# Kernel optimization log

Measured on AMD Instinct MI355X. Metric: run time of the kernel, lower is better.

## Reference

```python
import jax, jax.numpy as jnp
import numpy as np

GAMMAS = (0.01, 0.1, 1.0, 10.0, 100.0)
FOCAL_GAMMA = 2.0
SMOOTH = 0.1
TASK_W = (0.4, 0.3, 0.3)
A_RECON, A_ORTH, A_ADV = 1.0, 0.1, 0.1
NUM_DOMAINS = 4
NUM_LABELS1 = 4


def focal_smooth(logits, targets, maskf):
    # FocalLoss.forward with smoothing > 0, masked mean
    n_classes = logits.shape[1]
    log_p = jax.nn.log_softmax(logits, axis=1)
    p = jnp.exp(log_p)
    onehot = jax.nn.one_hot(targets, n_classes, dtype=logits.dtype)
    smooth = onehot * (1.0 - SMOOTH) + SMOOTH / n_classes
    ce = -(smooth * log_p).sum(axis=1)
    pt = jnp.take_along_axis(p, targets[:, None], axis=1)[:, 0]
    loss = ce * (1.0 - pt) ** FOCAL_GAMMA
    return (loss * maskf).sum() / jnp.maximum(maskf.sum(), 1.0)


def ce_masked(logits, targets, maskf):
    log_p = jax.nn.log_softmax(logits, axis=1)
    nll = -jnp.take_along_axis(log_p, targets[:, None], axis=1)[:, 0]
    return (nll * maskf).sum() / jnp.maximum(maskf.sum(), 1.0)


def cond_mmd(feats, domains, labels, maskf):
    # Global pairwise sq-distance matrix; multi-gamma RBF kernels summed.
    sq = (feats ** 2).sum(axis=-1)                      # (B,)
    Dmat = sq[:, None] + sq[None, :] - 2.0 * feats @ feats.T  # (B,B)
    Ksum = jnp.zeros_like(Dmat)
    for g in GAMMAS:
        Ksum = Ksum + jnp.exp(-g * Dmat)
    loss = jnp.asarray(0.0, feats.dtype)
    count = jnp.asarray(0.0, feats.dtype)
    for lab in range(NUM_LABELS1):
        lm = (labels == lab).astype(feats.dtype) * maskf
        for d1 in range(NUM_DOMAINS):
            m1 = lm * (domains == d1).astype(feats.dtype)
            n1 = m1.sum()
            Km1 = Ksum @ m1
            for d2 in range(d1 + 1, NUM_DOMAINS):
                m2 = lm * (domains == d2).astype(feats.dtype)
                n2 = m2.sum()
                valid = (n1 > 1) & (n2 > 1)
                term = (m1 @ Km1) / jnp.maximum(n1, 1.0) ** 2 \
                     + (m2 @ (Ksum @ m2)) / jnp.maximum(n2, 1.0) ** 2 \
                     - 2.0 * (m2 @ Km1) / jnp.maximum(n1 * n2, 1.0)
                loss = loss + jnp.where(valid, term, 0.0)
                count = count + valid.astype(feats.dtype)
    return loss / jnp.maximum(count, 1.0)


def hsic(c, s):
    n = c.shape[0]
    c = c / jnp.maximum(jnp.linalg.norm(c, axis=-1, keepdims=True), 1e-12)
    s = s / jnp.maximum(jnp.linalg.norm(s, axis=-1, keepdims=True), 1e-12)
    K = c @ c.T
    L = s @ s.T
    Kc = K - K.mean(axis=0, keepdims=True) - K.mean(axis=1, keepdims=True) + K.mean()
    Lc = L - L.mean(axis=0, keepdims=True) - L.mean(axis=1, keepdims=True) + L.mean()
    return (Kc * Lc).sum() / (n - 1) ** 2


def setup_inputs() -> dict:
    key = jax.random.key(0)
    ks = jax.random.split(key, 20)
    B, D, H = 4096, 256, 768
    inp = {
        'logits1': jax.random.normal(ks[0], (B, 4), jnp.float32),
        'labels1': jax.random.randint(ks[1], (B,), 0, 4),
        'logits2': jax.random.normal(ks[2], (B, 6), jnp.float32),
        'labels2': jax.random.randint(ks[3], (B,), 0, 6),
        'logits3': jax.random.normal(ks[4], (B, 3), jnp.float32),
        'labels3': jax.random.randint(ks[5], (B,), 0, 3),
        'c_v': jax.random.normal(ks[6], (B, D), jnp.float32),
        's_v': jax.random.normal(ks[7], (B, D), jnp.float32),
        'c_t': jax.random.normal(ks[8], (B, D), jnp.float32),
        's_t': jax.random.normal(ks[9], (B, D), jnp.float32),
        'v_sv': jax.random.normal(ks[10], (B, NUM_DOMAINS), jnp.float32),
        'v_st': jax.random.normal(ks[11], (B, NUM_DOMAINS), jnp.float32),
        'domain_labels': jax.random.randint(ks[12], (B,), 0, NUM_DOMAINS),
        'mask': jnp.ones((B,), dtype=bool),
        'h_img_recon': jax.random.normal(ks[13], (B, H), jnp.float32),
        'h_img_orig': jax.random.normal(ks[14], (B, H), jnp.float32),
        'h_txt_recon': jax.random.normal(ks[15], (B, H), jnp.float32),
        'h_txt_orig': jax.random.normal(ks[16], (B, H), jnp.float32),
    }
    return inp


def reference(logits1, labels1, logits2, labels2, logits3, labels3,
              c_v, s_v, c_t, s_t, v_sv, v_st, domain_labels, mask,
              h_img_recon, h_img_orig, h_txt_recon, h_txt_orig):
    maskf = mask.astype(jnp.float32)
    total = jnp.asarray(0.0, jnp.float32)
    # classification (focal + label smoothing), per-task weighted
    total = total + TASK_W[0] * focal_smooth(logits1, labels1, maskf)
    total = total + TASK_W[1] * focal_smooth(logits2, labels2, maskf)
    total = total + TASK_W[2] * focal_smooth(logits3, labels3, maskf)
    # adversarial: CE on spurious domain logits + conditional MMD on causal feats
    l_adv_s = ce_masked(v_sv, domain_labels, maskf) + ce_masked(v_st, domain_labels, maskf)
    l_adv_c = cond_mmd(c_v, domain_labels, labels1, maskf) \
            + cond_mmd(c_t, domain_labels, labels1, maskf)
    total = total + A_ADV * (l_adv_s + l_adv_c)
    # orthogonality (HSIC), on unmasked features as in source
    l_orth = hsic(c_v, s_v) + hsic(c_t, s_t)
    total = total + A_ORTH * l_orth
    # reconstruction MSE
    l_recon = jnp.mean((h_img_recon - h_img_orig) ** 2) + jnp.mean((h_txt_recon - h_txt_orig) ** 2)
    total = total + A_RECON * l_recon
    return total
```

## Files before the change

### kernel.cpp

```cpp
#include <hip/hip_runtime.h>
#include <hip/hip_bf16.h>


typedef short bf16x8 __attribute__((ext_vector_type(8)));
typedef float f32x4 __attribute__((ext_vector_type(4)));
typedef unsigned long long u64;
typedef unsigned int u32;

static constexpr int D = 256;
static constexpr int H = 768;
static constexpr int NG = 16;
static constexpr float FX32 = 4294967296.f;
static constexpr float IFX32 = 2.3283064365386963e-10f;

__device__ inline void gAddFx(u64* p, float v) {
  long long q = (long long)llroundf(v * FX32);
  atomicAdd(p, (u64)q);
}
__device__ inline float fxToF(u64 v) { return (float)(long long)v * IFX32; }

__device__ inline float focal_n(const float* x, int n, int tgt,
                                float s_over_n, float oms) {
  float mx = x[0];
  for (int c = 1; c < n; ++c) mx = fmaxf(mx, x[c]);
  float se = 0.f, sx = 0.f;
  for (int c = 0; c < n; ++c) { se += __expf(x[c] - mx); sx += x[c]; }
  float logZ = mx + __logf(se);
  float ce = logZ - oms * x[tgt] - s_over_n * sx;
  float pt = __expf(x[tgt] - logZ);
  float om = 1.f - pt;
  return ce * om * om;
}

extern "C" __global__ __launch_bounds__(256) void k_pre(
    const void* __restrict__ mask, const int* __restrict__ y1,
    const int* __restrict__ dom,
    const float* __restrict__ l1, const float* __restrict__ l2,
    const float* __restrict__ l3, const int* __restrict__ y2,
    const int* __restrict__ y3,
    const float* __restrict__ vsv, const float* __restrict__ vst,
    const float* __restrict__ cv, const float* __restrict__ sv,
    const float* __restrict__ ct, const float* __restrict__ st,
    const float* __restrict__ ir, const float* __restrict__ io,
    const float* __restrict__ trc, const float* __restrict__ to,
    u64* SA, u64* GCU, u64* U64,
    int* gid, float* sq, float* inv, unsigned short* bf, u32* CNTB,
    int B, int N4, int NA, int NB) {
  __shared__ u32 sh3[3];
  __shared__ u32 cnt[17];
  __shared__ int redi[4];
  __shared__ float redf[4];
  __shared__ float redf5[5][4];
  __shared__ float ub[4][64][4];
  int bid = blockIdx.x;
  int t = threadIdx.x;

  if (bid < NA) {
    if (t < 3) sh3[t] = 0;
    if (t < 17) cnt[t] = 0;
    __syncthreads();
    u32 a = 0, b2 = 0, cd = 0;
    if (t * 16 + 15 < B) {
      uint4 wv = ((const uint4*)mask)[t];
      u32 ws[4] = {wv.x, wv.y, wv.z, wv.w};
      #pragma unroll
      for (int j = 0; j < 4; ++j) {
        a |= ws[j] & 0xffu; b2 |= ws[j] & 0xff00u; cd |= ws[j] & 0xffff0000u;
      }
    }
    if (a) atomicOr(&sh3[0], 1u);
    if (b2) atomicOr(&sh3[1], 1u);
    if (cd) atomicOr(&sh3[2], 1u);
    __syncthreads();
    int mode;
    if ((sh3[1] | sh3[2]) == 0) mode = 0;
    else if (sh3[0] == 0 && sh3[1] == 0) mode = 1;
    else mode = 2;
    int r = bid * 256 + t;
    int mi = 0;
    float s[5] = {0.f, 0.f, 0.f, 0.f, 0.f};
    if (r < B) {
      if (mode == 0)      mi = ((const int*)mask)[r] ? 1 : 0;
      else if (mode == 1) mi = (((const float*)mask)[r] != 0.f) ? 1 : 0;
      else                mi = ((const unsigned char*)mask)[r] ? 1 : 0;
      int g = -1;
      if (mi) { g = y1[r] * 4 + dom[r]; atomicAdd(&cnt[g], 1u); }
      else atomicAdd(&cnt[16], 1u);
      gid[r] = g;
      if (mi) {
        float x[6];
        for (int c = 0; c < 4; ++c) x[c] = l1[r * 4 + c];
        s[0] = focal_n(x, 4, y1[r], 0.1f / 4.f, 0.9f);
        for (int c = 0; c < 6; ++c) x[c] = l2[r * 6 + c];
        s[1] = focal_n(x, 6, y2[r], 0.1f / 6.f, 0.9f);
        for (int c = 0; c < 3; ++c) x[c] = l3[r * 3 + c];
        s[2] = focal_n(x, 3, y3[r], 0.1f / 3.f, 0.9f);
        int d = dom[r];
        for (int c = 0; c < 4; ++c) x[c] = vsv[r * 4 + c];
        {
          float mx = fmaxf(fmaxf(x[0], x[1]), fmaxf(x[2], x[3]));
          float se = __expf(x[0]-mx)+__expf(x[1]-mx)+__expf(x[2]-mx)+__expf(x[3]-mx);
          s[3] = mx + __logf(se) - x[d];
        }
        for (int c = 0; c < 4; ++c) x[c] = vst[r * 4 + c];
        {
          float mx = fmaxf(fmaxf(x[0], x[1]), fmaxf(x[2], x[3]));
          float se = __expf(x[0]-mx)+__expf(x[1]-mx)+__expf(x[2]-mx)+__expf(x[3]-mx);
          s[4] = mx + __logf(se) - x[d];
        }
      }
    }
    int v = mi;
    #pragma unroll
    for (int o = 32; o > 0; o >>= 1) {
      v += __shfl_down(v, o);
      #pragma unroll
      for (int k = 0; k < 5; ++k) s[k] += __shfl_down(s[k], o);
    }
    if ((t & 63) == 0) {
      redi[t >> 6] = v;
      #pragma unroll
      for (int k = 0; k < 5; ++k) redf5[k][t >> 6] = s[k];
    }
    __syncthreads();
    if (t == 0) {
      atomicAdd(&SA[5], (u64)(redi[0] + redi[1] + redi[2] + redi[3]));
      #pragma unroll
      for (int k = 0; k < 5; ++k)
        gAddFx(&SA[k], redf5[k][0] + redf5[k][1] + redf5[k][2] + redf5[k][3]);
    }
    if (t < NG && cnt[t]) atomicAdd(&GCU[t], (u64)cnt[t]);
    if (t < 17) CNTB[bid * 17 + t] = cnt[t];
  } else if (bid < NA + NB) {
    int b = bid - NA;
    int perF = NB >> 2;
    int f = b / perF;
    int rb = b - f * perF;
    const float* p = (f == 0) ? cv : (f == 1) ? sv : (f == 2) ? ct : st;
    int w = t >> 6, L = t & 63;
    float up0 = 0.f, up1 = 0.f, up2 = 0.f, up3 = 0.f;
    for (int bt = 0; bt < 2; ++bt) {
      int rbase = rb * 32 + w * 8 + bt * 4;
      float4 vv[4];
      #pragma unroll
      for (int i = 0; i < 4; ++i)
        vv[i] = ((const float4*)(p + (size_t)(rbase + i) * D))[L];
      float ss[4];
      #pragma unroll
      for (int i = 0; i < 4; ++i)
        ss[i] = vv[i].x * vv[i].x + vv[i].y * vv[i].y
              + vv[i].z * vv[i].z + vv[i].w * vv[i].w;
      #pragma unroll
      for (int o = 32; o > 0; o >>= 1) {
        #pragma unroll
        for (int i = 0; i < 4; ++i) ss[i] += __shfl_down(ss[i], o);
      }
      #pragma unroll
      for (int i = 0; i < 4; ++i) ss[i] = __shfl(ss[i], 0);
      #pragma unroll
      for (int i = 0; i < 4; ++i) {
        int r = rbase + i;
        float iv = 1.f / fmaxf(sqrtf(ss[i]), 1e-12f);
        if ((f & 1) == 0) {
          int fi = f >> 1;
          alignas(8) __hip_bfloat16 hb[4];
          hb[0] = __float2bfloat16(vv[i].x); hb[1] = __float2bfloat16(vv[i].y);
          hb[2] = __float2bfloat16(vv[i].z); hb[3] = __float2bfloat16(vv[i].w);
          *(uint2*)(bf + ((size_t)fi * B + r) * D + L * 4) = *(uint2*)hb;
          if (L == 0) sq[fi * B + r] = ss[i];
        }
        if (L == 0) inv[f * B + r] = iv;
        up0 += vv[i].x * iv; up1 += vv[i].y * iv;
        up2 += vv[i].z * iv; up3 += vv[i].w * iv;
      }
    }
    ub[w][L][0] = up0; ub[w][L][1] = up1; ub[w][L][2] = up2; ub[w][L][3] = up3;
    __syncthreads();
    if (t < 64) {
      u64* Uf = U64 + f * D + 4 * t;
      #pragma unroll
      for (int j = 0; j < 4; ++j) {
        float s4 = ub[0][t][j] + ub[1][t][j] + ub[2][t][j] + ub[3][t][j];
        gAddFx(Uf + j, s4);
      }
    }
  } else {
    int cidx = bid - (NA + NB);
    int j = cidx >> 9;
    int cb = cidx & 511;
    const float4* A  = (const float4*)(j ? trc : ir);
    const float4* Bp = (const float4*)(j ? to : io);
    int CH = (N4 + 511) >> 9;
    int base = cb * CH;
    int end = min(base + CH, N4);
    float acc = 0.f;
    int idx = base + t;
    for (; idx + 256 < end; idx += 512) {
      float4 a0 = A[idx],       b0 = Bp[idx];
      float4 a1 = A[idx + 256], b1 = Bp[idx + 256];
      float dx0 = a0.x-b0.x, dy0 = a0.y-b0.y, dz0 = a0.z-b0.z, dw0 = a0.w-b0.w;
      float dx1 = a1.x-b1.x, dy1 = a1.y-b1.y, dz1 = a1.z-b1.z, dw1 = a1.w-b1.w;
      acc += dx0*dx0 + dy0*dy0 + dz0*dz0 + dw0*dw0
           + dx1*dx1 + dy1*dy1 + dz1*dz1 + dw1*dw1;
    }
    if (idx < end) {
      float4 a = A[idx], b = Bp[idx];
      float dx = a.x-b.x, dy = a.y-b.y, dz = a.z-b.z, dw = a.w-b.w;
      acc += dx*dx + dy*dy + dz*dz + dw*dw;
    }
    #pragma unroll
    for (int o = 32; o > 0; o >>= 1) acc += __shfl_down(acc, o);
    if ((t & 63) == 0) redf[t >> 6] = acc;
    __syncthreads();
    if (t == 0) gAddFx(&SA[6 + j], redf[0] + redf[1] + redf[2] + redf[3]);
  }
}

extern "C" __global__ __launch_bounds__(256) void k_mid(
    const u32* __restrict__ CNTB, const int* __restrict__ gid,
    const float* __restrict__ sq,
    const float* __restrict__ cv, const float* __restrict__ sv,
    const float* __restrict__ ct, const float* __restrict__ st,
    const float* __restrict__ inv,
    int* __restrict__ perm, float* __restrict__ sqp, int* __restrict__ OFF,
    unsigned short* __restrict__ bnT, int B, int NA) {
  __shared__ float ld[64 * 65];
  __shared__ u32 cbs[17], tots[17], wcnt[4][17];
  __shared__ u32 base[18];
  int b = blockIdx.x, t = threadIdx.x;

  if (b < NA) {
    if (t < 68) ((u32*)wcnt)[t] = 0;
    if (t < 17) {
      u32 cb = 0, tot = 0;
      for (int b2 = 0; b2 < NA; ++b2) {
        u32 c = CNTB[b2 * 17 + t];
        cb += (b2 < b) ? c : 0u;
        tot += c;
      }
      cbs[t] = cb; tots[t] = tot;
    }
    int r = b * 256 + t;
    int g = 16;
    if (r < B) { int gg = gid[r]; g = (gg < 0) ? 16 : gg; }
    __syncthreads();
    if (t == 0) {
      u32 s = 0;
      for (int g2 = 0; g2 < 17; ++g2) { base[g2] = s; s += tots[g2]; }
      base[17] = s;
    }
    u64 msk = ~0ull;
    #pragma unroll
    for (int bit = 0; bit < 5; ++bit) {
      int bv = (g >> bit) & 1;
      u64 bl = __ballot(bv);
      msk &= bv ? bl : ~bl;
    }
    int lane = t & 63, w = t >> 6;
    int rwave = __popcll(msk & ((1ull << lane) - 1ull));
    if (rwave == 0) wcnt[w][g] = (u32)__popcll(msk);
    __syncthreads();
    if (r < B) {
      int rank = rwave;
      for (int w2 = 0; w2 < 4; ++w2) if (w2 < w) rank += (int)wcnt[w2][g];
      int pos = (int)(base[g] + cbs[g]) + rank;
      perm[pos] = r;
      sqp[pos] = sq[r];
      sqp[B + pos] = sq[B + r];
    }
    if (b == 0 && t < 18) OFF[t] = (int)base[t];
  } else {
    int TPF = (B >> 6) * 4;
    int tb = b - NA;
    int fm = tb / TPF, tile = tb - fm * TPF;
    int it = tile >> 2, at = tile & 3;
    const float* src = (fm == 0) ? cv : (fm == 1) ? sv : (fm == 2) ? ct : st;
    const float* ivf = inv + (size_t)fm * B;
    int i0 = it * 64, a0 = at * 64;
    for (int e = t; e < 1024; e += 256) {
      int i = e >> 4, c4 = e & 15;
      float4 v = ((const float4*)(src + (size_t)(i0 + i) * D))[at * 16 + c4];
      float ivv = ivf[i0 + i];
      ld[i * 65 + c4 * 4 + 0] = v.x * ivv;
      ld[i * 65 + c4 * 4 + 1] = v.y * ivv;
      ld[i * 65 + c4 * 4 + 2] = v.z * ivv;
      ld[i * 65 + c4 * 4 + 3] = v.w * ivv;
    }
    __syncthreads();
    unsigned short* dst = bnT + (size_t)fm * D * B;
    for (int e = t; e < 512; e += 256) {
      int a = e >> 3, ic = e & 7;
      alignas(16) unsigned short h[8];
      #pragma unroll
      for (int j = 0; j < 8; ++j) {
        __hip_bfloat16 hb = __float2bfloat16(ld[(ic * 8 + j) * 65 + a]);
        h[j] = *(unsigned short*)&hb;
      }
      *(uint4*)(dst + (size_t)(a0 + a) * B + i0 + ic * 8) = *(uint4*)h;
    }
  }
}

extern "C" __global__ __launch_bounds__(256) void k_big(
    const unsigned short* __restrict__ bf, const float* __restrict__ sqp,
    const int* __restrict__ perm, const int* __restrict__ OFF,
    const unsigned short* __restrict__ bnT, float* __restrict__ Mf32,
    u64* GSP, int B) {
  __shared__ __align__(16) char smem[17536];
  unsigned short* Ab = (unsigned short*)smem;
  unsigned short* Bb = (unsigned short*)(smem + 8192);
  int bid = blockIdx.x;
  int tid = threadIdx.x;
  int w = tid >> 6, L = tid & 63, m = L & 15, q = L >> 4;
  int r0 = tid >> 3, ck = tid & 7;
  int swz = (ck ^ (r0 & 7)) * 8;
  int ar = w * 16 + m;

  if (bid < 64) {
    int half = bid & 1, bb = (bid >> 1) & 3, ab = (bid >> 3) & 3, p = (bid >> 5) & 1;
    const unsigned short* Abase = bnT + (size_t)(2 * p) * D * B;
    const unsigned short* Bbase = bnT + (size_t)(2 * p + 1) * D * B;
    size_t kof = (size_t)half * (B >> 1) + ck * 8;
    const uint4* gA0 = (const uint4*)(Abase + (size_t)(ab * 64 + r0) * B + kof);
    const uint4* gA1 = (const uint4*)(Abase + (size_t)(ab * 64 + r0 + 32) * B + kof);
    const uint4* gB0 = (const uint4*)(Bbase + (size_t)(bb * 64 + r0) * B + kof);
    const uint4* gB1 = (const uint4*)(Bbase + (size_t)(bb * 64 + r0 + 32) * B + kof);
    uint4* dA0 = (uint4*)&Ab[r0 * 64 + swz];
    uint4* dA1 = (uint4*)&Ab[(r0 + 32) * 64 + swz];
    uint4* dB0 = (uint4*)&Bb[r0 * 64 + swz];
    uint4* dB1 = (uint4*)&Bb[(r0 + 32) * 64 + swz];
    f32x4 acc[4] = {{0.f,0.f,0.f,0.f},{0.f,0.f,0.f,0.f},
                    {0.f,0.f,0.f,0.f},{0.f,0.f,0.f,0.f}};
    int nh = B >> 7;
    for (int hq = 0; hq < nh; ++hq) {
      *dA0 = gA0[hq * 8]; *dA1 = gA1[hq * 8];
      *dB0 = gB0[hq * 8]; *dB1 = gB1[hq * 8];
      __syncthreads();
      #pragma unroll
      for (int kk = 0; kk < 2; ++kk) {
        bf16x8 aF = *(const bf16x8*)&Ab[ar * 64 + (((kk * 4 + q) ^ (ar & 7)) * 8)];
        #pragma unroll
        for (int c = 0; c < 4; ++c) {
          int br = c * 16 + m;
          bf16x8 bF = *(const bf16x8*)&Bb[br * 64 + (((kk * 4 + q) ^ (br & 7)) * 8)];
          acc[c] = __builtin_amdgcn_mfma_f32_16x16x32_bf16(aF, bF, acc[c], 0, 0, 0);
        }
      }
      if (hq < nh - 1) __syncthreads();
    }
    float* Mo = Mf32 + (size_t)(half * 2 + p) * D * D;
    int ri0 = w * 16 + q * 4;
    #pragma unroll
    for (int c = 0; c < 4; ++c) {
      #pragma unroll
      for (int v = 0; v < 4; ++v)
        Mo[(size_t)(ab * 64 + ri0 + v) * D + bb * 64 + c * 16 + m] = acc[c][v];
    }
    return;
  }

  float* sA = (float*)(smem + 16384);
  float* sB = (float*)(smem + 16640);
  int*   pA = (int*)(smem + 16896);
  int*   pB = (int*)(smem + 17152);
  int*   offs = (int*)(smem + 17408);

  int idx2 = bid - 64;
  int feat = idx2 & 1;
  int tlin = idx2 >> 1;
  int NT = B / 64;
  float tf = (float)tlin;
  int ti = (int)((2.f * NT + 1.f -
                  sqrtf((2.f * NT + 1.f) * (2.f * NT + 1.f) - 8.f * tf)) * 0.5f);
  while (ti > 0 && (ti * NT - (ti * (ti - 1)) / 2) > tlin) --ti;
  while (((ti + 1) * NT - ((ti + 1) * ti) / 2) <= tlin) ++ti;
  int tj = ti + (tlin - (ti * NT - (ti * (ti - 1)) / 2));
  int i0 = ti * 64, j0 = tj * 64;
  bool diag = (ti == tj);
  const unsigned short* fb = bf + (size_t)feat * B * D;
  const float* sqf = sqp + (size_t)feat * B;

  if (tid < 64) { pA[tid] = perm[i0 + tid]; sA[tid] = sqf[i0 + tid]; }
  else if (tid < 128) { int r = tid - 64; pB[r] = perm[j0 + r]; sB[r] = sqf[j0 + r]; }
  else if (tid < 146) offs[tid - 128] = OFF[tid - 128];
  __syncthreads();

  int gr0 = 0, nbr = 0, gc0 = 0, ncb = 0;
  #pragma unroll
  for (int g = 1; g <= 17; ++g) {
    int o = offs[g];
    gr0 += (o <= i0) ? 1 : 0;
    nbr += (o > i0 && o < i0 + 64) ? 1 : 0;
    gc0 += (o <= j0) ? 1 : 0;
    ncb += (o > j0 && o < j0 + 64) ? 1 : 0;
  }
  if (gr0 == 16 || gc0 == 16) return;
  int gr1 = gr0 + nbr;
  int gc1 = gc0 + ncb;
  int s_r = nbr ? offs[gr1] : i0 + 64;
  int s_c = ncb ? offs[gc1] : j0 + 64;

  const uint4* gA0 = (const uint4*)(fb + (size_t)pA[r0] * D + ck * 8);
  const uint4* gA1 = (const uint4*)(fb + (size_t)pA[r0 + 32] * D + ck * 8);
  uint4* dA0 = (uint4*)&Ab[r0 * 64 + swz];
  uint4* dA1 = (uint4*)&Ab[(r0 + 32) * 64 + swz];
  const uint4* gB0 = nullptr; const uint4* gB1 = nullptr;
  uint4* dB0 = nullptr; uint4* dB1 = nullptr;
  if (!diag) {
    gB0 = (const uint4*)(fb + (size_t)pB[r0] * D + ck * 8);
    gB1 = (const uint4*)(fb + (size_t)pB[r0 + 32] * D + ck * 8);
    dB0 = (uint4*)&Bb[r0 * 64 + swz];
    dB1 = (uint4*)&Bb[(r0 + 32) * 64 + swz];
  }
  const unsigned short* Bp = diag ? Ab : Bb;

  f32x4 acc[4] = {{0.f,0.f,0.f,0.f},{0.f,0.f,0.f,0.f},
                  {0.f,0.f,0.f,0.f},{0.f,0.f,0.f,0.f}};

  for (int hq = 0; hq < 4; ++hq) {
    *dA0 = gA0[hq * 8]; *dA1 = gA1[hq * 8];
    if (!diag) { *dB0 = gB0[hq * 8]; *dB1 = gB1[hq * 8]; }
    __syncthreads();
    #pragma unroll
    for (int kk = 0; kk < 2; ++kk) {
      bf16x8 aF = *(const bf16x8*)&Ab[ar * 64 + (((kk * 4 + q) ^ (ar & 7)) * 8)];
      #pragma unroll
      for (int c = 0; c < 4; ++c) {
        int br = c * 16 + m;
        bf16x8 bF = *(const bf16x8*)&Bp[br * 64 + (((kk * 4 + q) ^ (br & 7)) * 8)];
        acc[c] = __builtin_amdgcn_mfma_f32_16x16x32_bf16(aF, bF, acc[c], 0, 0, 0);
      }
    }
    if (hq < 3) __syncthreads();
  }

  int ri0 = w * 16 + q * 4;
  u64* gsp = GSP + ((size_t)(tlin & 63) * 2 + feat) * NG * NG;

  if (nbr <= 1 && ncb <= 1) {
    float siv[4]; bool rhiv[4];
    #pragma unroll
    for (int v = 0; v < 4; ++v) {
      siv[v] = sA[ri0 + v];
      rhiv[v] = (i0 + ri0 + v) >= s_r;
    }
    float a00 = 0.f, a01 = 0.f, a10 = 0.f, a11 = 0.f;
    #pragma unroll
    for (int c = 0; c < 4; ++c) {
      int rj = c * 16 + m;
      float sb = sB[rj];
      float lo = 0.f, hi = 0.f;
      #pragma unroll
      for (int v = 0; v < 4; ++v) {
        float d = fmaxf(siv[v] + sb - 2.f * acc[c][v], 0.f);
        float K = __expf(-0.01f * d) + __expf(-0.1f * d) + __expf(-d)
                + __expf(-10.f * d) + __expf(-100.f * d);
        if (diag) {
          int ri = ri0 + v;
          K = (ri > rj) ? 0.f : (ri == rj) ? 5.f : K;
        }
        float kh = rhiv[v] ? K : 0.f;
        hi += kh; lo += K - kh;
      }
      bool chi = (j0 + rj) >= s_c;
      float loH = chi ? lo : 0.f;
      float hiH = chi ? hi : 0.f;
      a00 += lo - loH; a01 += loH;
      a10 += hi - hiH; a11 += hiH;
    }
    #pragma unroll
    for (int o = 32; o > 0; o >>= 1) {
      a00 += __shfl_down(a00, o); a01 += __shfl_down(a01, o);
      a10 += __shfl_down(a10, o); a11 += __shfl_down(a11, o);
    }
    if (L == 0) {
      if (a00 != 0.f)
        atomicAdd(&gsp[gr0 * NG + gc0], (u64)(long long)llroundf(a00 * 65536.f));
      if (a01 != 0.f && gc1 < 16)
        atomicAdd(&gsp[gr0 * NG + gc1], (u64)(long long)llroundf(a01 * 65536.f));
      if (a10 != 0.f && gr1 < 16)
        atomicAdd(&gsp[gr1 * NG + gc0], (u64)(long long)llroundf(a10 * 65536.f));
      if (a11 != 0.f && gr1 < 16 && gc1 < 16)
        atomicAdd(&gsp[gr1 * NG + gc1], (u64)(long long)llroundf(a11 * 65536.f));
    }
  } else {
    int giv[4]; float siv[4];
    #pragma unroll
    for (int v = 0; v < 4; ++v) {
      int idx = i0 + ri0 + v;
      int g = 0;
      #pragma unroll
      for (int k = 1; k <= 16; ++k) g += (offs[k] <= idx) ? 1 : 0;
      giv[v] = g;
      siv[v] = sA[ri0 + v];
    }
    #pragma unroll
    for (int c = 0; c < 4; ++c) {
      int rj = c * 16 + m;
      int jdx = j0 + rj;
      int gj = 0;
      #pragma unroll
      for (int k = 1; k <= 16; ++k) gj += (offs[k] <= jdx) ? 1 : 0;
      float sb = sB[rj];
      #pragma unroll
      for (int v = 0; v < 4; ++v) {
        int ri = ri0 + v;
        if (giv[v] < 16 && gj < 16 && !(diag && ri > rj)) {
          float K;
          if (diag && ri == rj) K = 5.f;
          else {
            float d = fmaxf(siv[v] + sb - 2.f * acc[c][v], 0.f);
            K = __expf(-0.01f * d) + __expf(-0.1f * d) + __expf(-d)
              + __expf(-10.f * d) + __expf(-100.f * d);
          }
          u32 kf = (u32)(K * 65536.f + 0.5f);
          atomicAdd(&gsp[giv[v] * NG + gj], (u64)kf);
        }
      }
    }
  }
}

extern "C" __global__ __launch_bounds__(256) void k_hsic(
    const u64* __restrict__ U64, const float* __restrict__ Mf32, u64* SA) {
  __shared__ float red[8];
  __shared__ float ush[32], vsh[D];
  int p = blockIdx.y;
  int k0 = blockIdx.x * 32;
  int t = threadIdx.x;
  vsh[t] = fxToF(U64[(2 * p + 1) * D + t]);
  if (t < 32) ush[t] = fxToF(U64[(2 * p) * D + k0 + t]);
  __syncthreads();
  const float* M0 = Mf32 + (size_t)p * D * D;
  const float* M1 = Mf32 + (size_t)(2 + p) * D * D;
  float trkl = 0.f, cr = 0.f;
  #pragma unroll 4
  for (int k = 0; k < 32; ++k) {
    float mv = M0[(size_t)(k0 + k) * D + t] + M1[(size_t)(k0 + k) * D + t];
    trkl += mv * mv;
    cr += ush[k] * mv;
  }
  cr *= vsh[t];
  #pragma unroll
  for (int o = 32; o > 0; o >>= 1) { trkl += __shfl_down(trkl, o); cr += __shfl_down(cr, o); }
  if ((t & 63) == 0) { red[t >> 6] = trkl; red[4 + (t >> 6)] = cr; }
  __syncthreads();
  if (t == 0) gAddFx(&SA[10 + p], red[0] + red[1] + red[2] + red[3]);
  if (t == 64) gAddFx(&SA[12 + p], red[4] + red[5] + red[6] + red[7]);
}

extern "C" __global__ __launch_bounds__(256) void k_final(
    const u64* SA, const u64* GCU, const u64* GSP,
    const u64* U64, float* out, int B) {
  __shared__ float red[8];
  __shared__ float gssh[2 * NG * NG];
  int t = threadIdx.x;
  for (int e = t; e < 2 * NG * NG; e += 256) {
    u64 ssum = 0;
    int f = e >> 8, idx = e & 255;
    for (int cpy = 0; cpy < 64; ++cpy)
      ssum += GSP[((size_t)cpy * 2 + f) * NG * NG + idx];
    gssh[e] = (float)((double)ssum * (1.0 / 65536.0));
  }
  __syncthreads();

  float n = (float)B;
  float hs[2];
  for (int p = 0; p < 2; ++p) {
    float ut = fxToF(U64[(2 * p) * D + t]);
    float vt = fxToF(U64[(2 * p + 1) * D + t]);
    float uu = ut * ut, vv = vt * vt;
    #pragma unroll
    for (int o = 32; o > 0; o >>= 1) { uu += __shfl_down(uu, o); vv += __shfl_down(vv, o); }
    __syncthreads();
    if ((t & 63) == 0) { red[t >> 6] = uu; red[4 + (t >> 6)] = vv; }
    __syncthreads();
    float uus = red[0] + red[1] + red[2] + red[3];
    float vvs = red[4] + red[5] + red[6] + red[7];
    float trkl = (float)((double)(long long)SA[10 + p] * (double)IFX32);
    float cr   = (float)((double)(long long)SA[12 + p] * (double)IFX32);
    hs[p] = (trkl - (2.f / n) * cr + uus * vvs / (n * n))
          / ((n - 1.f) * (n - 1.f));
    __syncthreads();
  }
  if (t == 0) {
    float msum = fmaxf((float)SA[5], 1.f);
    float f1 = fxToF(SA[0]) / msum;
    float f2 = fxToF(SA[1]) / msum;
    float f3 = fxToF(SA[2]) / msum;
    float cesv = fxToF(SA[3]) / msum;
    float cest = fxToF(SA[4]) / msum;
    float mmd[2];
    for (int f = 0; f < 2; ++f) {
      float loss = 0.f, cntv = 0.f;
      for (int lab = 0; lab < 4; ++lab)
        for (int d1 = 0; d1 < 4; ++d1)
          for (int d2 = d1 + 1; d2 < 4; ++d2) {
            int a = lab * 4 + d1, b = lab * 4 + d2;
            float n1 = (float)GCU[a], n2 = (float)GCU[b];
            if (n1 > 1.f && n2 > 1.f) {
              float g11 = 2.f * gssh[f * 256 + a * NG + a] - 5.f * n1;
              float g22 = 2.f * gssh[f * 256 + b * NG + b] - 5.f * n2;
              float g12 = gssh[f * 256 + a * NG + b];
              loss += g11 / (fmaxf(n1, 1.f) * fmaxf(n1, 1.f))
                    + g22 / (fmaxf(n2, 1.f) * fmaxf(n2, 1.f))
                    - 2.f * g12 / fmaxf(n1 * n2, 1.f);
              cntv += 1.f;
            }
          }
      mmd[f] = loss / fmaxf(cntv, 1.f);
    }
    double rs = ((double)(long long)SA[6] + (double)(long long)SA[7])
              * (double)IFX32;
    float recon = (float)(rs / ((double)B * (double)H));
    float total = 0.4f * f1 + 0.3f * f2 + 0.3f * f3
                + 0.1f * (cesv + cest + mmd[0] + mmd[1])
                + 0.1f * (hs[0] + hs[1])
                + recon;
    out[0] = total;
  }
}

extern "C" void kernel_launch(void* const* d_in, const int* in_sizes, int n_in,
                              void* d_out, int out_size, void* d_ws, size_t ws_size,
                              hipStream_t stream) {
  const float* l1  = (const float*)d_in[0];
  const int*   y1  = (const int*)d_in[1];
  const float* l2  = (const float*)d_in[2];
  const int*   y2  = (const int*)d_in[3];
  const float* l3  = (const float*)d_in[4];
  const int*   y3  = (const int*)d_in[5];
  const float* cv  = (const float*)d_in[6];
  const float* sv  = (const float*)d_in[7];
  const float* ct  = (const float*)d_in[8];
  const float* st  = (const float*)d_in[9];
  const float* vsv = (const float*)d_in[10];
  const float* vst = (const float*)d_in[11];
  const int*   dom = (const int*)d_in[12];
  const void*  mask= d_in[13];
  const float* ir  = (const float*)d_in[14];
  const float* io  = (const float*)d_in[15];
  const float* trc = (const float*)d_in[16];
  const float* to  = (const float*)d_in[17];
  int B = in_sizes[1];

  u64* SA  = (u64*)d_ws;
  u64* GCU = SA + 32;
  u64* U64 = GCU + 16;
  u64* GSP = U64 + 4 * D;
  u64* zend = GSP + 64 * 2 * NG * NG;
  size_t zeroBytes = (size_t)((char*)zend - (char*)d_ws);
  unsigned short* bf  = (unsigned short*)zend;
  unsigned short* bnT = bf + 2 * (size_t)B * D;
  float* Mf32 = (float*)(bnT + 4 * (size_t)D * B);
  int*   gid = (int*)(Mf32 + 4 * (size_t)D * D);
  float* sq  = (float*)(gid + B);
  float* inv = sq + 2 * B;
  int*   perm = (int*)(inv + 4 * B);
  float* sqp  = (float*)(perm + B);
  int*   OFF  = (int*)(sqp + 2 * B);
  u32*   CNTB = (u32*)(OFF + 18);

  int NA = B / 256;
  int NB = B / 8;
  int NC = 1024;
  int N4 = B * H / 4;

  hipMemsetAsync(d_ws, 0, zeroBytes, stream);
  k_pre<<<NA + NB + NC, 256, 0, stream>>>(
      mask, y1, dom, l1, l2, l3, y2, y3, vsv, vst,
      cv, sv, ct, st, ir, io, trc, to,
      SA, GCU, U64, gid, sq, inv, bf, CNTB, B, N4, NA, NB);
  int NTR = B / 4;
  k_mid<<<NA + NTR, 256, 0, stream>>>(CNTB, gid, sq, cv, sv, ct, st, inv,
                                      perm, sqp, OFF, bnT, B, NA);
  int NT = B / 64;
  int nmmd = 2 * (NT * (NT + 1) / 2);
  k_big<<<64 + nmmd, 256, 0, stream>>>(bf, sqp, perm, OFF, bnT, Mf32, GSP, B);
  k_hsic<<<dim3(8, 2), 256, 0, stream>>>(U64, Mf32, SA);
  k_final<<<1, 256, 0, stream>>>(SA, GCU, GSP, U64, (float*)d_out, B);
}
```

Before: 207.9 us.

## Merge pre/mid and hsic/final kernels via global flags, split HSIC K four ways

Folds k_mid into k_pre and k_hsic into k_final, replacing kernel boundaries with atomic-counter release/acquire spin-waits, which removes two launches. The HSIC cross-covariance GEMM now splits K four ways (128 blocks) to expose more parallelism, and both GEMM paths prefetch the next global tile into registers while computing. The norm stage loads 8 rows at once. The spin-waits assume the producer blocks get scheduled before the consumers and can deadlock if they do not. The extra partial matrices also add workspace traffic.

```diff
diff --git a/kernel.cpp b/kernel.cpp
--- a/kernel.cpp
+++ b/kernel.cpp
@@ -18,6 +18,15 @@
   atomicAdd(p, (u64)q);
 }
 __device__ inline float fxToF(u64 v) { return (float)(long long)v * IFX32; }
+
+__device__ inline void flagRelease(u64* f) {
+  __threadfence();
+  atomicAdd(f, 1ull);
+}
+__device__ inline void flagAcquire(u64* f, u64 n) {
+  while (atomicAdd(f, 0ull) < n) __builtin_amdgcn_s_sleep(8);
+  __threadfence();
+}
 
 __device__ inline float focal_n(const float* x, int n, int tgt,
                                 float s_over_n, float oms) {
@@ -45,6 +54,7 @@
     const float* __restrict__ trc, const float* __restrict__ to,
     u64* SA, u64* GCU, u64* U64,
     int* gid, float* sq, float* inv, unsigned short* bf, u32* CNTB,
+    int* perm, float* sqp, int* OFF, unsigned short* bnT, u64* FLG,
     int B, int N4, int NA, int NB) {
   __shared__ u32 sh3[3];
   __shared__ u32 cnt[17];
@@ -52,8 +62,12 @@
   __shared__ float redf[4];
   __shared__ float redf5[5][4];
   __shared__ float ub[4][64][4];
+  __shared__ float ld[64 * 65];
+  __shared__ u32 cbs[17], tots[17], wcnt[4][17];
+  __shared__ u32 sbase[18];
   int bid = blockIdx.x;
   int t = threadIdx.x;
+  int NC = 1024;
 
   if (bid < NA) {
     if (t < 3) sh3[t] = 0;
@@ -131,6 +145,8 @@
     }
     if (t < NG && cnt[t]) atomicAdd(&GCU[t], (u64)cnt[t]);
     if (t < 17) CNTB[bid * 17 + t] = cnt[t];
+    __syncthreads();
+    if (t == 0) flagRelease(&FLG[0]);
   } else if (bid < NA + NB) {
     int b = bid - NA;
     int perF = NB >> 2;
@@ -138,41 +154,39 @@
     int rb = b - f * perF;
     const float* p = (f == 0) ? cv : (f == 1) ? sv : (f == 2) ? ct : st;
     int w = t >> 6, L = t & 63;
+    int rbase = rb * 32 + w * 8;
+    float4 vv[8];
+    #pragma unroll
+    for (int i = 0; i < 8; ++i)
+      vv[i] = ((const float4*)(p + (size_t)(rbase + i) * D))[L];
+    float ss[8];
+    #pragma unroll
+    for (int i = 0; i < 8; ++i)
+      ss[i] = vv[i].x * vv[i].x + vv[i].y * vv[i].y
+            + vv[i].z * vv[i].z + vv[i].w * vv[i].w;
+    #pragma unroll
+    for (int o = 32; o > 0; o >>= 1) {
+      #pragma unroll
+      for (int i = 0; i < 8; ++i) ss[i] += __shfl_down(ss[i], o);
+    }
+    #pragma unroll
+    for (int i = 0; i < 8; ++i) ss[i] = __shfl(ss[i], 0);
     float up0 = 0.f, up1 = 0.f, up2 = 0.f, up3 = 0.f;
-    for (int bt = 0; bt < 2; ++bt) {
-      int rbase = rb * 32 + w * 8 + bt * 4;
-      float4 vv[4];
-      #pragma unroll
-      for (int i = 0; i < 4; ++i)
-        vv[i] = ((const float4*)(p + (size_t)(rbase + i) * D))[L];
-      float ss[4];
-      #pragma unroll
-      for (int i = 0; i < 4; ++i)
-        ss[i] = vv[i].x * vv[i].x + vv[i].y * vv[i].y
-              + vv[i].z * vv[i].z + vv[i].w * vv[i].w;
-      #pragma unroll
-      for (int o = 32; o > 0; o >>= 1) {
-        #pragma unroll
-        for (int i = 0; i < 4; ++i) ss[i] += __shfl_down(ss[i], o);
-      }
-      #pragma unroll
-      for (int i = 0; i < 4; ++i) ss[i] = __shfl(ss[i], 0);
-      #pragma unroll
-      for (int i = 0; i < 4; ++i) {
-        int r = rbase + i;
-        float iv = 1.f / fmaxf(sqrtf(ss[i]), 1e-12f);
-        if ((f & 1) == 0) {
-          int fi = f >> 1;
-          alignas(8) __hip_bfloat16 hb[4];
-          hb[0] = __float2bfloat16(vv[i].x); hb[1] = __float2bfloat16(vv[i].y);
-          hb[2] = __float2bfloat16(vv[i].z); hb[3] = __float2bfloat16(vv[i].w);
-          *(uint2*)(bf + ((size_t)fi * B + r) * D + L * 4) = *(uint2*)hb;
-          if (L == 0) sq[fi * B + r] = ss[i];
-        }
-        if (L == 0) inv[f * B + r] = iv;
-        up0 += vv[i].x * iv; up1 += vv[i].y * iv;
-        up2 += vv[i].z * iv; up3 += vv[i].w * iv;
-      }
+    #pragma unroll
+    for (int i = 0; i < 8; ++i) {
+      int r = rbase + i;
+      float iv = 1.f / fmaxf(sqrtf(ss[i]), 1e-12f);
+      if ((f & 1) == 0) {
+        int fi = f >> 1;
+        alignas(8) __hip_bfloat16 hb[4];
+        hb[0] = __float2bfloat16(vv[i].x); hb[1] = __float2bfloat16(vv[i].y);
+        hb[2] = __float2bfloat16(vv[i].z); hb[3] = __float2bfloat16(vv[i].w);
+        *(uint2*)(bf + ((size_t)fi * B + r) * D + L * 4) = *(uint2*)hb;
+        if (L == 0) sq[fi * B + r] = ss[i];
+      }
+      if (L == 0) inv[f * B + r] = iv;
+      up0 += vv[i].x * iv; up1 += vv[i].y * iv;
+      up2 += vv[i].z * iv; up3 += vv[i].w * iv;
     }
     ub[w][L][0] = up0; ub[w][L][1] = up1; ub[w][L][2] = up2; ub[w][L][3] = up3;
     __syncthreads();
@@ -184,7 +198,9 @@
         gAddFx(Uf + j, s4);
       }
     }
-  } else {
+    __syncthreads();
+    if (t == 0) flagRelease(&FLG[1]);
+  } else if (bid < NA + NB + NC) {
     int cidx = bid - (NA + NB);
     int j = cidx >> 9;
     int cb = cidx & 511;
@@ -213,23 +229,13 @@
     if ((t & 63) == 0) redf[t >> 6] = acc;
     __syncthreads();
     if (t == 0) gAddFx(&SA[6 + j], redf[0] + redf[1] + redf[2] + redf[3]);
-  }
-}
-
-extern "C" __global__ __launch_bounds__(256) void k_mid(
-    const u32* __restrict__ CNTB, const int* __restrict__ gid,
-    const float* __restrict__ sq,
-    const float* __restrict__ cv, const float* __restrict__ sv,
-    const float* __restrict__ ct, const float* __restrict__ st,
-    const float* __restrict__ inv,
-    int* __restrict__ perm, float* __restrict__ sqp, int* __restrict__ OFF,
-    unsigned short* __restrict__ bnT, int B, int NA) {
-  __shared__ float ld[64 * 65];
-  __shared__ u32 cbs[17], tots[17], wcnt[4][17];
-  __shared__ u32 base[18];
-  int b = blockIdx.x, t = threadIdx.x;
-
-  if (b < NA) {
+  } else if (bid < NA + NB + NC + NA) {
+    if (t == 0) {
+      flagAcquire(&FLG[0], (u64)NA);
+      flagAcquire(&FLG[1], (u64)NB);
+    }
+    __syncthreads();
+    int b = bid - (NA + NB + NC);
     if (t < 68) ((u32*)wcnt)[t] = 0;
     if (t < 17) {
       u32 cb = 0, tot = 0;
@@ -246,8 +252,8 @@
     __syncthreads();
     if (t == 0) {
       u32 s = 0;
-      for (int g2 = 0; g2 < 17; ++g2) { base[g2] = s; s += tots[g2]; }
-      base[17] = s;
+      for (int g2 = 0; g2 < 17; ++g2) { sbase[g2] = s; s += tots[g2]; }
+      sbase[17] = s;
     }
     u64 msk = ~0ull;
     #pragma unroll
@@ -263,15 +269,17 @@
     if (r < B) {
       int rank = rwave;
       for (int w2 = 0; w2 < 4; ++w2) if (w2 < w) rank += (int)wcnt[w2][g];
-      int pos = (int)(base[g] + cbs[g]) + rank;
+      int pos = (int)(sbase[g] + cbs[g]) + rank;
       perm[pos] = r;
       sqp[pos] = sq[r];
       sqp[B + pos] = sq[B + r];
     }
-    if (b == 0 && t < 18) OFF[t] = (int)base[t];
+    if (b == 0 && t < 18) OFF[t] = (int)sbase[t];
   } else {
+    if (t == 0) flagAcquire(&FLG[1], (u64)NB);
+    __syncthreads();
     int TPF = (B >> 6) * 4;
-    int tb = b - NA;
+    int tb = bid - (NA + NB + NC + NA);
     int fm = tb / TPF, tile = tb - fm * TPF;
     int it = tile >> 2, at = tile & 3;
     const float* src = (fm == 0) ? cv : (fm == 1) ? sv : (fm == 2) ? ct : st;
@@ -316,11 +324,11 @@
   int swz = (ck ^ (r0 & 7)) * 8;
   int ar = w * 16 + m;
 
-  if (bid < 64) {
-    int half = bid & 1, bb = (bid >> 1) & 3, ab = (bid >> 3) & 3, p = (bid >> 5) & 1;
+  if (bid < 128) {
+    int ks = bid & 3, bb = (bid >> 2) & 3, ab = (bid >> 4) & 3, p = (bid >> 6) & 1;
     const unsigned short* Abase = bnT + (size_t)(2 * p) * D * B;
     const unsigned short* Bbase = bnT + (size_t)(2 * p + 1) * D * B;
-    size_t kof = (size_t)half * (B >> 1) + ck * 8;
+    size_t kof = (size_t)ks * (B >> 2) + ck * 8;
     const uint4* gA0 = (const uint4*)(Abase + (size_t)(ab * 64 + r0) * B + kof);
     const uint4* gA1 = (const uint4*)(Abase + (size_t)(ab * 64 + r0 + 32) * B + kof);
     const uint4* gB0 = (const uint4*)(Bbase + (size_t)(bb * 64 + r0) * B + kof);
@@ -331,11 +339,15 @@
     uint4* dB1 = (uint4*)&Bb[(r0 + 32) * 64 + swz];
     f32x4 acc[4] = {{0.f,0.f,0.f,0.f},{0.f,0.f,0.f,0.f},
                     {0.f,0.f,0.f,0.f},{0.f,0.f,0.f,0.f}};
-    int nh = B >> 7;
+    int nh = B >> 8;
+    uint4 rA0 = gA0[0], rA1 = gA1[0], rB0 = gB0[0], rB1 = gB1[0];
     for (int hq = 0; hq < nh; ++hq) {
-      *dA0 = gA0[hq * 8]; *dA1 = gA1[hq * 8];
-      *dB0 = gB0[hq * 8]; *dB1 = gB1[hq * 8];
+      *dA0 = rA0; *dA1 = rA1; *dB0 = rB0; *dB1 = rB1;
       __syncthreads();
+      if (hq < nh - 1) {
+        rA0 = gA0[(hq + 1) * 8]; rA1 = gA1[(hq + 1) * 8];
+        rB0 = gB0[(hq + 1) * 8]; rB1 = gB1[(hq + 1) * 8];
+      }
       #pragma unroll
       for (int kk = 0; kk < 2; ++kk) {
         bf16x8 aF = *(const bf16x8*)&Ab[ar * 64 + (((kk * 4 + q) ^ (ar & 7)) * 8)];
@@ -348,7 +360,7 @@
       }
       if (hq < nh - 1) __syncthreads();
     }
-    float* Mo = Mf32 + (size_t)(half * 2 + p) * D * D;
+    float* Mo = Mf32 + (size_t)(ks * 2 + p) * D * D;
     int ri0 = w * 16 + q * 4;
     #pragma unroll
     for (int c = 0; c < 4; ++c) {
@@ -365,7 +377,7 @@
   int*   pB = (int*)(smem + 17152);
   int*   offs = (int*)(smem + 17408);
 
-  int idx2 = bid - 64;
+  int idx2 = bid - 128;
   int feat = idx2 & 1;
   int tlin = idx2 >> 1;
   int NT = B / 64;
@@ -404,23 +416,28 @@
   const uint4* gA1 = (const uint4*)(fb + (size_t)pA[r0 + 32] * D + ck * 8);
   uint4* dA0 = (uint4*)&Ab[r0 * 64 + swz];
   uint4* dA1 = (uint4*)&Ab[(r0 + 32) * 64 + swz];
-  const uint4* gB0 = nullptr; const uint4* gB1 = nullptr;
-  uint4* dB0 = nullptr; uint4* dB1 = nullptr;
+  const uint4* gB0 = gA0; const uint4* gB1 = gA1;
+  uint4* dB0 = (uint4*)&Bb[r0 * 64 + swz];
+  uint4* dB1 = (uint4*)&Bb[(r0 + 32) * 64 + swz];
   if (!diag) {
     gB0 = (const uint4*)(fb + (size_t)pB[r0] * D + ck * 8);
     gB1 = (const uint4*)(fb + (size_t)pB[r0 + 32] * D + ck * 8);
-    dB0 = (uint4*)&Bb[r0 * 64 + swz];
-    dB1 = (uint4*)&Bb[(r0 + 32) * 64 + swz];
   }
   const unsigned short* Bp = diag ? Ab : Bb;
 
   f32x4 acc[4] = {{0.f,0.f,0.f,0.f},{0.f,0.f,0.f,0.f},
                   {0.f,0.f,0.f,0.f},{0.f,0.f,0.f,0.f}};
 
+  uint4 rA0 = gA0[0], rA1 = gA1[0], rB0, rB1;
+  if (!diag) { rB0 = gB0[0]; rB1 = gB1[0]; }
   for (int hq = 0; hq < 4; ++hq) {
-    *dA0 = gA0[hq * 8]; *dA1 = gA1[hq * 8];
-    if (!diag) { *dB0 = gB0[hq * 8]; *dB1 = gB1[hq * 8]; }
-    __syncthreads();
+    *dA0 = rA0; *dA1 = rA1;
+    if (!diag) { *dB0 = rB0; *dB1 = rB1; }
+    __syncthreads();
+    if (hq < 3) {
+      rA0 = gA0[(hq + 1) * 8]; rA1 = gA1[(hq + 1) * 8];
+      if (!diag) { rB0 = gB0[(hq + 1) * 8]; rB1 = gB1[(hq + 1) * 8]; }
+    }
     #pragma unroll
     for (int kk = 0; kk < 2; ++kk) {
       bf16x8 aF = *(const bf16x8*)&Ab[ar * 64 + (((kk * 4 + q) ^ (ar & 7)) * 8)];
@@ -521,40 +538,48 @@
   }
 }
 
-extern "C" __global__ __launch_bounds__(256) void k_hsic(
-    const u64* __restrict__ U64, const float* __restrict__ Mf32, u64* SA) {
+extern "C" __global__ __launch_bounds__(256) void k_fin(
+    const u64* __restrict__ U64, const float* __restrict__ Mf32,
+    u64* SA, const u64* __restrict__ GCU, const u64* __restrict__ GSP,
+    float* out, u64* FLG, int B) {
   __shared__ float red[8];
   __shared__ float ush[32], vsh[D];
-  int p = blockIdx.y;
-  int k0 = blockIdx.x * 32;
+  __shared__ float gssh[2 * NG * NG];
+  int bid = blockIdx.x;
   int t = threadIdx.x;
-  vsh[t] = fxToF(U64[(2 * p + 1) * D + t]);
-  if (t < 32) ush[t] = fxToF(U64[(2 * p) * D + k0 + t]);
+
+  if (bid < 16) {
+    int p = bid >> 3;
+    int k0 = (bid & 7) * 32;
+    vsh[t] = fxToF(U64[(2 * p + 1) * D + t]);
+    if (t < 32) ush[t] = fxToF(U64[(2 * p) * D + k0 + t]);
+    __syncthreads();
+    const float* M0 = Mf32 + (size_t)(0 * 2 + p) * D * D;
+    const float* M1 = Mf32 + (size_t)(1 * 2 + p) * D * D;
+    const float* M2 = Mf32 + (size_t)(2 * 2 + p) * D * D;
+    const float* M3 = Mf32 + (size_t)(3 * 2 + p) * D * D;
+    float trkl = 0.f, cr = 0.f;
+    #pragma unroll 4
+    for (int k = 0; k < 32; ++k) {
+      size_t off = (size_t)(k0 + k) * D + t;
+      float mv = M0[off] + M1[off] + M2[off] + M3[off];
+      trkl += mv * mv;
+      cr += ush[k] * mv;
+    }
+    cr *= vsh[t];
+    #pragma unroll
+    for (int o = 32; o > 0; o >>= 1) { trkl += __shfl_down(trkl, o); cr += __shfl_down(cr, o); }
+    if ((t & 63) == 0) { red[t >> 6] = trkl; red[4 + (t >> 6)] = cr; }
+    __syncthreads();
+    if (t == 0) gAddFx(&SA[10 + p], red[0] + red[1] + red[2] + red[3]);
+    if (t == 64) gAddFx(&SA[12 + p], red[4] + red[5] + red[6] + red[7]);
+    __syncthreads();
+    if (t == 0) flagRelease(&FLG[2]);
+    return;
+  }
+
+  if (t == 0) flagAcquire(&FLG[2], 16ull);
   __syncthreads();
-  const float* M0 = Mf32 + (size_t)p * D * D;
-  const float* M1 = Mf32 + (size_t)(2 + p) * D * D;
-  float trkl = 0.f, cr = 0.f;
-  #pragma unroll 4
-  for (int k = 0; k < 32; ++k) {
-    float mv = M0[(size_t)(k0 + k) * D + t] + M1[(size_t)(k0 + k) * D + t];
-    trkl += mv * mv;
-    cr += ush[k] * mv;
-  }
-  cr *= vsh[t];
-  #pragma unroll
-  for (int o = 32; o > 0; o >>= 1) { trkl += __shfl_down(trkl, o); cr += __shfl_down(cr, o); }
-  if ((t & 63) == 0) { red[t >> 6] = trkl; red[4 + (t >> 6)] = cr; }
-  __syncthreads();
-  if (t == 0) gAddFx(&SA[10 + p], red[0] + red[1] + red[2] + red[3]);
-  if (t == 64) gAddFx(&SA[12 + p], red[4] + red[5] + red[6] + red[7]);
-}
-
-extern "C" __global__ __launch_bounds__(256) void k_final(
-    const u64* SA, const u64* GCU, const u64* GSP,
-    const u64* U64, float* out, int B) {
-  __shared__ float red[8];
-  __shared__ float gssh[2 * NG * NG];
-  int t = threadIdx.x;
   for (int e = t; e < 2 * NG * NG; e += 256) {
     u64 ssum = 0;
     int f = e >> 8, idx = e & 255;
@@ -648,12 +673,13 @@
   u64* GCU = SA + 32;
   u64* U64 = GCU + 16;
   u64* GSP = U64 + 4 * D;
-  u64* zend = GSP + 64 * 2 * NG * NG;
+  u64* FLG = GSP + 64 * 2 * NG * NG;
+  u64* zend = FLG + 4;
   size_t zeroBytes = (size_t)((char*)zend - (char*)d_ws);
   unsigned short* bf  = (unsigned short*)zend;
   unsigned short* bnT = bf + 2 * (size_t)B * D;
   float* Mf32 = (float*)(bnT + 4 * (size_t)D * B);
-  int*   gid = (int*)(Mf32 + 4 * (size_t)D * D);
+  int*   gid = (int*)(Mf32 + 8 * (size_t)D * D);
   float* sq  = (float*)(gid + B);
   float* inv = sq + 2 * B;
   int*   perm = (int*)(inv + 4 * B);
@@ -664,19 +690,17 @@
   int NA = B / 256;
   int NB = B / 8;
   int NC = 1024;
+  int NTR = B / 4;
   int N4 = B * H / 4;
 
   hipMemsetAsync(d_ws, 0, zeroBytes, stream);
-  k_pre<<<NA + NB + NC, 256, 0, stream>>>(
+  k_pre<<<NA + NB + NC + NA + NTR, 256, 0, stream>>>(
       mask, y1, dom, l1, l2, l3, y2, y3, vsv, vst,
       cv, sv, ct, st, ir, io, trc, to,
-      SA, GCU, U64, gid, sq, inv, bf, CNTB, B, N4, NA, NB);
-  int NTR = B / 4;
-  k_mid<<<NA + NTR, 256, 0, stream>>>(CNTB, gid, sq, cv, sv, ct, st, inv,
-                                      perm, sqp, OFF, bnT, B, NA);
+      SA, GCU, U64, gid, sq, inv, bf, CNTB,
+      perm, sqp, OFF, bnT, FLG, B, N4, NA, NB);
   int NT = B / 64;
   int nmmd = 2 * (NT * (NT + 1) / 2);
-  k_big<<<64 + nmmd, 256, 0, stream>>>(bf, sqp, perm, OFF, bnT, Mf32, GSP, B);
-  k_hsic<<<dim3(8, 2), 256, 0, stream>>>(U64, Mf32, SA);
-  k_final<<<1, 256, 0, stream>>>(SA, GCU, GSP, U64, (float*)d_out, B);
+  k_big<<<128 + nmmd, 256, 0, stream>>>(bf, sqp, perm, OFF, bnT, Mf32, GSP, B);
+  k_fin<<<17, 256, 0, stream>>>(U64, Mf32, SA, GCU, GSP, (float*)d_out, FLG, B);
 }
```

Result: slower. 283.5 us (+36.4%).

## Split HSIC GEMM K-range four ways and register-prefetch tiles in k_big

Applied to the files above, without the earlier changes.

The HSIC cross-covariance GEMM blocks now split the K (batch) dimension into four slices instead of two, doubling block count and writing four partial matrices that k_hsic sums. Both the HSIC GEMM and MMD tile loops now prefetch the next global tile into registers before computing on the current LDS tile, overlapping global loads with MFMA work. The normalization blocks in k_pre load all 8 rows at once instead of two batches of 4. This trades extra partial-matrix memory and k_hsic reads for more parallelism and latency hiding.

```diff
diff --git a/kernel.cpp b/kernel.cpp
--- a/kernel.cpp
+++ b/kernel.cpp
@@ -138,41 +138,39 @@
     int rb = b - f * perF;
     const float* p = (f == 0) ? cv : (f == 1) ? sv : (f == 2) ? ct : st;
     int w = t >> 6, L = t & 63;
+    int rbase = rb * 32 + w * 8;
+    float4 vv[8];
+    #pragma unroll
+    for (int i = 0; i < 8; ++i)
+      vv[i] = ((const float4*)(p + (size_t)(rbase + i) * D))[L];
+    float ss[8];
+    #pragma unroll
+    for (int i = 0; i < 8; ++i)
+      ss[i] = vv[i].x * vv[i].x + vv[i].y * vv[i].y
+            + vv[i].z * vv[i].z + vv[i].w * vv[i].w;
+    #pragma unroll
+    for (int o = 32; o > 0; o >>= 1) {
+      #pragma unroll
+      for (int i = 0; i < 8; ++i) ss[i] += __shfl_down(ss[i], o);
+    }
+    #pragma unroll
+    for (int i = 0; i < 8; ++i) ss[i] = __shfl(ss[i], 0);
     float up0 = 0.f, up1 = 0.f, up2 = 0.f, up3 = 0.f;
-    for (int bt = 0; bt < 2; ++bt) {
-      int rbase = rb * 32 + w * 8 + bt * 4;
-      float4 vv[4];
-      #pragma unroll
-      for (int i = 0; i < 4; ++i)
-        vv[i] = ((const float4*)(p + (size_t)(rbase + i) * D))[L];
-      float ss[4];
-      #pragma unroll
-      for (int i = 0; i < 4; ++i)
-        ss[i] = vv[i].x * vv[i].x + vv[i].y * vv[i].y
-              + vv[i].z * vv[i].z + vv[i].w * vv[i].w;
-      #pragma unroll
-      for (int o = 32; o > 0; o >>= 1) {
-        #pragma unroll
-        for (int i = 0; i < 4; ++i) ss[i] += __shfl_down(ss[i], o);
-      }
-      #pragma unroll
-      for (int i = 0; i < 4; ++i) ss[i] = __shfl(ss[i], 0);
-      #pragma unroll
-      for (int i = 0; i < 4; ++i) {
-        int r = rbase + i;
-        float iv = 1.f / fmaxf(sqrtf(ss[i]), 1e-12f);
-        if ((f & 1) == 0) {
-          int fi = f >> 1;
-          alignas(8) __hip_bfloat16 hb[4];
-          hb[0] = __float2bfloat16(vv[i].x); hb[1] = __float2bfloat16(vv[i].y);
-          hb[2] = __float2bfloat16(vv[i].z); hb[3] = __float2bfloat16(vv[i].w);
-          *(uint2*)(bf + ((size_t)fi * B + r) * D + L * 4) = *(uint2*)hb;
-          if (L == 0) sq[fi * B + r] = ss[i];
-        }
-        if (L == 0) inv[f * B + r] = iv;
-        up0 += vv[i].x * iv; up1 += vv[i].y * iv;
-        up2 += vv[i].z * iv; up3 += vv[i].w * iv;
-      }
+    #pragma unroll
+    for (int i = 0; i < 8; ++i) {
+      int r = rbase + i;
+      float iv = 1.f / fmaxf(sqrtf(ss[i]), 1e-12f);
+      if ((f & 1) == 0) {
+        int fi = f >> 1;
+        alignas(8) __hip_bfloat16 hb[4];
+        hb[0] = __float2bfloat16(vv[i].x); hb[1] = __float2bfloat16(vv[i].y);
+        hb[2] = __float2bfloat16(vv[i].z); hb[3] = __float2bfloat16(vv[i].w);
+        *(uint2*)(bf + ((size_t)fi * B + r) * D + L * 4) = *(uint2*)hb;
+        if (L == 0) sq[fi * B + r] = ss[i];
+      }
+      if (L == 0) inv[f * B + r] = iv;
+      up0 += vv[i].x * iv; up1 += vv[i].y * iv;
+      up2 += vv[i].z * iv; up3 += vv[i].w * iv;
     }
     ub[w][L][0] = up0; ub[w][L][1] = up1; ub[w][L][2] = up2; ub[w][L][3] = up3;
     __syncthreads();
@@ -316,11 +314,11 @@
   int swz = (ck ^ (r0 & 7)) * 8;
   int ar = w * 16 + m;
 
-  if (bid < 64) {
-    int half = bid & 1, bb = (bid >> 1) & 3, ab = (bid >> 3) & 3, p = (bid >> 5) & 1;
+  if (bid < 128) {
+    int ks = bid & 3, bb = (bid >> 2) & 3, ab = (bid >> 4) & 3, p = (bid >> 6) & 1;
     const unsigned short* Abase = bnT + (size_t)(2 * p) * D * B;
     const unsigned short* Bbase = bnT + (size_t)(2 * p + 1) * D * B;
-    size_t kof = (size_t)half * (B >> 1) + ck * 8;
+    size_t kof = (size_t)ks * (B >> 2) + ck * 8;
     const uint4* gA0 = (const uint4*)(Abase + (size_t)(ab * 64 + r0) * B + kof);
     const uint4* gA1 = (const uint4*)(Abase + (size_t)(ab * 64 + r0 + 32) * B + kof);
     const uint4* gB0 = (const uint4*)(Bbase + (size_t)(bb * 64 + r0) * B + kof);
@@ -331,11 +329,15 @@
     uint4* dB1 = (uint4*)&Bb[(r0 + 32) * 64 + swz];
     f32x4 acc[4] = {{0.f,0.f,0.f,0.f},{0.f,0.f,0.f,0.f},
                     {0.f,0.f,0.f,0.f},{0.f,0.f,0.f,0.f}};
-    int nh = B >> 7;
+    int nh = B >> 8;
+    uint4 rA0 = gA0[0], rA1 = gA1[0], rB0 = gB0[0], rB1 = gB1[0];
     for (int hq = 0; hq < nh; ++hq) {
-      *dA0 = gA0[hq * 8]; *dA1 = gA1[hq * 8];
-      *dB0 = gB0[hq * 8]; *dB1 = gB1[hq * 8];
+      *dA0 = rA0; *dA1 = rA1; *dB0 = rB0; *dB1 = rB1;
       __syncthreads();
+      if (hq < nh - 1) {
+        rA0 = gA0[(hq + 1) * 8]; rA1 = gA1[(hq + 1) * 8];
+        rB0 = gB0[(hq + 1) * 8]; rB1 = gB1[(hq + 1) * 8];
+      }
       #pragma unroll
       for (int kk = 0; kk < 2; ++kk) {
         bf16x8 aF = *(const bf16x8*)&Ab[ar * 64 + (((kk * 4 + q) ^ (ar & 7)) * 8)];
@@ -348,7 +350,7 @@
       }
       if (hq < nh - 1) __syncthreads();
     }
-    float* Mo = Mf32 + (size_t)(half * 2 + p) * D * D;
+    float* Mo = Mf32 + (size_t)(ks * 2 + p) * D * D;
     int ri0 = w * 16 + q * 4;
     #pragma unroll
     for (int c = 0; c < 4; ++c) {
@@ -365,7 +367,7 @@
   int*   pB = (int*)(smem + 17152);
   int*   offs = (int*)(smem + 17408);
 
-  int idx2 = bid - 64;
+  int idx2 = bid - 128;
   int feat = idx2 & 1;
   int tlin = idx2 >> 1;
   int NT = B / 64;
@@ -404,23 +406,28 @@
   const uint4* gA1 = (const uint4*)(fb + (size_t)pA[r0 + 32] * D + ck * 8);
   uint4* dA0 = (uint4*)&Ab[r0 * 64 + swz];
   uint4* dA1 = (uint4*)&Ab[(r0 + 32) * 64 + swz];
-  const uint4* gB0 = nullptr; const uint4* gB1 = nullptr;
-  uint4* dB0 = nullptr; uint4* dB1 = nullptr;
+  const uint4* gB0 = gA0; const uint4* gB1 = gA1;
+  uint4* dB0 = (uint4*)&Bb[r0 * 64 + swz];
+  uint4* dB1 = (uint4*)&Bb[(r0 + 32) * 64 + swz];
   if (!diag) {
     gB0 = (const uint4*)(fb + (size_t)pB[r0] * D + ck * 8);
     gB1 = (const uint4*)(fb + (size_t)pB[r0 + 32] * D + ck * 8);
-    dB0 = (uint4*)&Bb[r0 * 64 + swz];
-    dB1 = (uint4*)&Bb[(r0 + 32) * 64 + swz];
   }
   const unsigned short* Bp = diag ? Ab : Bb;
 
   f32x4 acc[4] = {{0.f,0.f,0.f,0.f},{0.f,0.f,0.f,0.f},
                   {0.f,0.f,0.f,0.f},{0.f,0.f,0.f,0.f}};
 
+  uint4 rA0 = gA0[0], rA1 = gA1[0], rB0, rB1;
+  if (!diag) { rB0 = gB0[0]; rB1 = gB1[0]; }
   for (int hq = 0; hq < 4; ++hq) {
-    *dA0 = gA0[hq * 8]; *dA1 = gA1[hq * 8];
-    if (!diag) { *dB0 = gB0[hq * 8]; *dB1 = gB1[hq * 8]; }
-    __syncthreads();
+    *dA0 = rA0; *dA1 = rA1;
+    if (!diag) { *dB0 = rB0; *dB1 = rB1; }
+    __syncthreads();
+    if (hq < 3) {
+      rA0 = gA0[(hq + 1) * 8]; rA1 = gA1[(hq + 1) * 8];
+      if (!diag) { rB0 = gB0[(hq + 1) * 8]; rB1 = gB1[(hq + 1) * 8]; }
+    }
     #pragma unroll
     for (int kk = 0; kk < 2; ++kk) {
       bf16x8 aF = *(const bf16x8*)&Ab[ar * 64 + (((kk * 4 + q) ^ (ar & 7)) * 8)];
@@ -531,12 +538,15 @@
   vsh[t] = fxToF(U64[(2 * p + 1) * D + t]);
   if (t < 32) ush[t] = fxToF(U64[(2 * p) * D + k0 + t]);
   __syncthreads();
-  const float* M0 = Mf32 + (size_t)p * D * D;
-  const float* M1 = Mf32 + (size_t)(2 + p) * D * D;
+  const float* M0 = Mf32 + (size_t)(0 * 2 + p) * D * D;
+  const float* M1 = Mf32 + (size_t)(1 * 2 + p) * D * D;
+  const float* M2 = Mf32 + (size_t)(2 * 2 + p) * D * D;
+  const float* M3 = Mf32 + (size_t)(3 * 2 + p) * D * D;
   float trkl = 0.f, cr = 0.f;
   #pragma unroll 4
   for (int k = 0; k < 32; ++k) {
-    float mv = M0[(size_t)(k0 + k) * D + t] + M1[(size_t)(k0 + k) * D + t];
+    size_t off = (size_t)(k0 + k) * D + t;
+    float mv = M0[off] + M1[off] + M2[off] + M3[off];
     trkl += mv * mv;
     cr += ush[k] * mv;
   }
@@ -653,7 +663,7 @@
   unsigned short* bf  = (unsigned short*)zend;
   unsigned short* bnT = bf + 2 * (size_t)B * D;
   float* Mf32 = (float*)(bnT + 4 * (size_t)D * B);
-  int*   gid = (int*)(Mf32 + 4 * (size_t)D * D);
+  int*   gid = (int*)(Mf32 + 8 * (size_t)D * D);
   float* sq  = (float*)(gid + B);
   float* inv = sq + 2 * B;
   int*   perm = (int*)(inv + 4 * B);
@@ -676,7 +686,7 @@
                                       perm, sqp, OFF, bnT, B, NA);
   int NT = B / 64;
   int nmmd = 2 * (NT * (NT + 1) / 2);
-  k_big<<<64 + nmmd, 256, 0, stream>>>(bf, sqp, perm, OFF, bnT, Mf32, GSP, B);
+  k_big<<<128 + nmmd, 256, 0, stream>>>(bf, sqp, perm, OFF, bnT, Mf32, GSP, B);
   k_hsic<<<dim3(8, 2), 256, 0, stream>>>(U64, Mf32, SA);
   k_final<<<1, 256, 0, stream>>>(SA, GCU, GSP, U64, (float*)d_out, B);
 }
```

After: 210.2 us. No clear change (+1.1%).
